# Kernel tuning notes

Hardware: AMD Instinct MI355X
Metric: run time of the kernel (lower is better)

Reference implementation:

```python
import jax, jax.numpy as jnp
import numpy as np

N = 8192
D = 512
N_SLICE = 64
K = 8
H = 30 * K  # 240


def _gen_k_slice(rng):
    xx = rng.normal(0.0, 1.0, (N_SLICE, K, D))
    slices = np.zeros((N_SLICE, K, D), dtype=np.float64)
    for i in range(N_SLICE):
        _, _, vh = np.linalg.svd(xx[i], full_matrices=False)
        slices[i] = vh
    return slices.astype(np.float32)


def setup_inputs() -> dict:
    key = jax.random.key(0)
    k1, k2, k3, k4, k5, k6, k7 = jax.random.split(key, 7)
    rng = np.random.default_rng(0)
    # conv weights: PyTorch Conv1d default init ~ U(-s, s), s = 1/sqrt(fan_in)
    s1 = 1.0 / np.sqrt(K)
    s3 = 1.0 / np.sqrt(H)
    return {
        "X": jax.random.normal(k1, (N, D), dtype=jnp.float32),
        "Y": jax.random.normal(k2, (N, D), dtype=jnp.float32),
        "X_noise": jax.random.normal(k3, (N, N_SLICE * K), dtype=jnp.float32),
        "thetas": jnp.asarray(_gen_k_slice(rng)),                     # [S, K, D]
        "W1": jax.random.uniform(k4, (N_SLICE, H, K), jnp.float32, -s1, s1),
        "b1": jax.random.uniform(k5, (N_SLICE, H), jnp.float32, -s1, s1),
        "W3": jax.random.uniform(k6, (N_SLICE, H), jnp.float32, -s3, s3),
        "b3": jax.random.uniform(k7, (N_SLICE,), jnp.float32, -s3, s3),
        "sigma_noise": 0,
    }


def _mlp(sample, W1, b1, W3, b3):
    # sample: [N, S, K] -> grouped 1x1 conv k->H, relu, grouped conv H->1
    h1 = jax.nn.relu(jnp.einsum('nsk,shk->nsh', sample, W1) + b1[None])
    return jnp.einsum('nsh,sh->ns', h1, W3) + b3[None]  # [N, S]


def reference(X, Y, X_noise, thetas, W1, b1, W3, b3, sigma_noise):
    # batched per-slice projections (fuses the n_slice matmul loop)
    x_sample = jnp.einsum('nd,skd->nsk', X, thetas)  # [N, S, K]
    y_sample = jnp.einsum('nd,skd->nsk', Y, thetas)
    if sigma_noise > 0:
        x_sample = x_sample + sigma_noise * X_noise.reshape(X.shape[0], N_SLICE, K)
    pred_x = _mlp(x_sample, W1, b1, W3, b3)  # [N, S]
    pred_y = _mlp(y_sample, W1, b1, W3, b3)
    n_y = pred_y.shape[0]
    ret = jnp.mean(pred_x, axis=0) - jax.nn.logsumexp(
        pred_y - jnp.log(jnp.float32(n_y)), axis=0)
    return jnp.mean(-ret)
```

## Files before the change

### kernel.cpp

```cpp
#include <hip/hip_runtime.h>
#include <hip/hip_bf16.h>

#define NROWS 8192
#define DDIM  512
#define NS    64
#define KK    8
#define HH    240
#define LDA   40
#define SP    136

typedef __attribute__((ext_vector_type(8))) short bf16x8;
typedef __attribute__((ext_vector_type(4))) float f32x4;

__device__ inline ushort f2bf(float x) {
    unsigned u = __float_as_uint(x);
    unsigned r = u + 0x7fffu + ((u >> 16) & 1u);
    return (ushort)(r >> 16);
}

__global__ __launch_bounds__(256)
void pack_w1_kernel(const float* __restrict__ W1, ushort* __restrict__ W1b)
{
    int i = (blockIdx.x * 256 + threadIdx.x) * 4;
    float4 v = *(const float4*)(W1 + i);
    ushort4 o;
    o.x = f2bf(v.x); o.y = f2bf(v.y); o.z = f2bf(v.z); o.w = f2bf(v.w);
    *(ushort4*)(W1b + i) = o;
}

__global__ __launch_bounds__(256, 4)
void proj_mlp_kernel(const float* __restrict__ X,
                     const float* __restrict__ Y,
                     const float* __restrict__ Xn,
                     const float* __restrict__ Th,
                     const ushort* __restrict__ W1b,
                     const float* __restrict__ b1,
                     const float* __restrict__ W3,
                     const float* __restrict__ b3,
                     const float* __restrict__ sig_p,
                     float* __restrict__ px,
                     float* __restrict__ py)
{
    __shared__ __align__(16) char smem[64 * SP * 2];
    ushort* aT = (ushort*)smem;
    ushort* bT = aT + 64 * LDA;
    ushort* sl = (ushort*)smem;

    const int tid  = threadIdx.x;
    const int w    = __builtin_amdgcn_readfirstlane(tid >> 6);
    const int lane = tid & 63;
    const int bx   = blockIdx.x;
    const int by   = blockIdx.y;

    const bool isX = (bx < 128);
    const int  bxl = isX ? bx : (bx - 128);
    const float* srcA = (isX ? X : Y) + (size_t)bxl * 64 * DDIM;
    const float* srcB = Th + (size_t)by * 128 * DDIM;

    f32x4 acc[2][4];
#pragma unroll
    for (int m = 0; m < 2; ++m)
#pragma unroll
        for (int n = 0; n < 4; ++n) acc[m][n] = (f32x4){0.f, 0.f, 0.f, 0.f};

    const int wr  = (w >> 1) * 32;
    const int wc  = (w & 1) * 64;
    const int r16 = lane & 15;
    const int hi4 = lane >> 4;
    const int offA = (wr + r16) * LDA + hi4 * 8;
    const int offB = (wc + r16) * LDA + hi4 * 8;

    float4 ra[2], rb[4];
#pragma unroll
    for (int i = 0; i < 2; ++i) {
        int f = tid + i * 256;
        ra[i] = *(const float4*)(srcA + (size_t)(f >> 3) * DDIM + (f & 7) * 4);
    }
#pragma unroll
    for (int i = 0; i < 4; ++i) {
        int f = tid + i * 256;
        rb[i] = *(const float4*)(srcB + (size_t)(f >> 3) * DDIM + (f & 7) * 4);
    }

#pragma unroll 1
    for (int kt = 0; kt < DDIM / 32; ++kt) {
        __syncthreads();
#pragma unroll
        for (int i = 0; i < 2; ++i) {
            int f = tid + i * 256;
            ushort4 o;
            o.x = f2bf(ra[i].x); o.y = f2bf(ra[i].y);
            o.z = f2bf(ra[i].z); o.w = f2bf(ra[i].w);
            *(ushort4*)(aT + (f >> 3) * LDA + (f & 7) * 4) = o;
        }
#pragma unroll
        for (int i = 0; i < 4; ++i) {
            int f = tid + i * 256;
            ushort4 o;
            o.x = f2bf(rb[i].x); o.y = f2bf(rb[i].y);
            o.z = f2bf(rb[i].z); o.w = f2bf(rb[i].w);
            *(ushort4*)(bT + (f >> 3) * LDA + (f & 7) * 4) = o;
        }
        __syncthreads();

        if (kt + 1 < DDIM / 32) {
            const int k0 = (kt + 1) * 32;
#pragma unroll
            for (int i = 0; i < 2; ++i) {
                int f = tid + i * 256;
                ra[i] = *(const float4*)(srcA + (size_t)(f >> 3) * DDIM + k0 + (f & 7) * 4);
            }
#pragma unroll
            for (int i = 0; i < 4; ++i) {
                int f = tid + i * 256;
                rb[i] = *(const float4*)(srcB + (size_t)(f >> 3) * DDIM + k0 + (f & 7) * 4);
            }
        }

        bf16x8 af[2], bf[4];
#pragma unroll
        for (int m = 0; m < 2; ++m) af[m] = *(const bf16x8*)(aT + offA + m * 16 * LDA);
#pragma unroll
        for (int n = 0; n < 4; ++n) bf[n] = *(const bf16x8*)(bT + offB + n * 16 * LDA);
#pragma unroll
        for (int m = 0; m < 2; ++m)
#pragma unroll
            for (int n = 0; n < 4; ++n)
                acc[m][n] = __builtin_amdgcn_mfma_f32_16x16x32_bf16(af[m], bf[n], acc[m][n], 0, 0, 0);
    }

    const float sig = *sig_p;
    const bool addnoise = (sig > 0.f) && isX;
    const int n0g = bxl * 64;

    __syncthreads();
#pragma unroll
    for (int m = 0; m < 2; ++m)
#pragma unroll
        for (int n = 0; n < 4; ++n) {
            int col = wc + n * 16 + r16;
#pragma unroll
            for (int j = 0; j < 4; ++j) {
                int row = wr + m * 16 + hi4 * 4 + j;
                float v = acc[m][n][j];
                if (addnoise)
                    v = fmaf(sig, Xn[(size_t)(n0g + row) * (NS * KK) + by * 128 + col], v);
                sl[row * SP + col] = f2bf(v);
            }
        }
    __syncthreads();

    float* dst = isX ? px : py;

#pragma unroll 1
    for (int si = 0; si < 4; ++si) {
        const int sloc = w * 4 + si;
        const int s    = by * 16 + sloc;

        bf16x8 a[4];
#pragma unroll
        for (int m = 0; m < 4; ++m) {
            bf16x8 t = {0, 0, 0, 0, 0, 0, 0, 0};
            if (lane < 16)
                t = *(const bf16x8*)(sl + (m * 16 + lane) * SP + sloc * 8);
            a[m] = t;
        }

        float pacc[4][4];
#pragma unroll
        for (int m = 0; m < 4; ++m)
#pragma unroll
            for (int j = 0; j < 4; ++j) pacc[m][j] = 0.f;

        const ushort* w1p = W1b + (size_t)s * HH * KK;
        const float*  b1p = b1 + s * HH;
        const float*  w3p = W3 + s * HH;

#pragma unroll 3
        for (int ht = 0; ht < HH / 16; ++ht) {
            const int h = ht * 16 + r16;
            bf16x8 bfr = {0, 0, 0, 0, 0, 0, 0, 0};
            if (lane < 16)
                bfr = *(const bf16x8*)(w1p + h * 8);
            const float b1v = b1p[h];
            const float w3v = w3p[h];
            const f32x4 z = (f32x4){b1v, b1v, b1v, b1v};
#pragma unroll
            for (int m = 0; m < 4; ++m) {
                f32x4 t = __builtin_amdgcn_mfma_f32_16x16x32_bf16(a[m], bfr, z, 0, 0, 0);
#pragma unroll
                for (int j = 0; j < 4; ++j)
                    pacc[m][j] = fmaf(fmaxf(t[j], 0.f), w3v, pacc[m][j]);
            }
        }

#pragma unroll
        for (int m = 0; m < 4; ++m)
#pragma unroll
            for (int j = 0; j < 4; ++j) {
                float v = pacc[m][j];
                v += __shfl_xor(v, 1);
                v += __shfl_xor(v, 2);
                v += __shfl_xor(v, 4);
                v += __shfl_xor(v, 8);
                pacc[m][j] = v;
            }

        const float b3v = b3[s];
        if (r16 == 0) {
#pragma unroll
            for (int m = 0; m < 4; ++m) {
                float4 o;
                o.x = pacc[m][0] + b3v;
                o.y = pacc[m][1] + b3v;
                o.z = pacc[m][2] + b3v;
                o.w = pacc[m][3] + b3v;
                *(float4*)(dst + (size_t)s * NROWS + n0g + m * 16 + hi4 * 4) = o;
            }
        }
    }
}

__global__ __launch_bounds__(256)
void reduce1_kernel(const float* __restrict__ px,
                    const float* __restrict__ py,
                    float4* __restrict__ part)
{
    const int s = blockIdx.x >> 2;
    const int q = blockIdx.x & 3;
    const int t = threadIdx.x;
    const float* prx = px + (size_t)s * NROWS + q * 2048;
    const float* pry = py + (size_t)s * NROWS + q * 2048;

    float sx = 0.f, m = -1e30f, se = 0.f;
#pragma unroll
    for (int i = 0; i < 8; ++i) {
        int idx = t + i * 256;
        sx += prx[idx];
        float v = pry[idx];
        if (v > m) {
            se = se * __expf(m - v) + 1.f;
            m = v;
        } else {
            se += __expf(v - m);
        }
    }

    __shared__ float smx[256], smm[256], sms[256];
    smx[t] = sx; smm[t] = m; sms[t] = se;
    __syncthreads();
    for (int off = 128; off > 0; off >>= 1) {
        if (t < off) {
            smx[t] += smx[t + off];
            float m1 = smm[t], m2 = smm[t + off];
            float mm = fmaxf(m1, m2);
            sms[t] = sms[t] * __expf(m1 - mm) + sms[t + off] * __expf(m2 - mm);
            smm[t] = mm;
        }
        __syncthreads();
    }
    if (t == 0) part[blockIdx.x] = (float4){smx[0], smm[0], sms[0], 0.f};
}

__global__ __launch_bounds__(64)
void final_kernel(const float4* __restrict__ part, float* __restrict__ out)
{
    const int s = threadIdx.x;
    float sum = 0.f, m = -1e30f, se = 0.f;
#pragma unroll
    for (int q = 0; q < 4; ++q) {
        float4 p = part[s * 4 + q];
        sum += p.x;
        float mm = fmaxf(m, p.y);
        se = se * __expf(m - mm) + p.z * __expf(p.y - mm);
        m = mm;
    }
    float lse  = m + logf(se);
    float term = lse - logf((float)NROWS) - sum / (float)NROWS;
#pragma unroll
    for (int off = 32; off > 0; off >>= 1) term += __shfl_down(term, off);
    if (s == 0) out[0] = term * (1.0f / (float)NS);
}

extern "C" void kernel_launch(void* const* d_in, const int* in_sizes, int n_in,
                              void* d_out, int out_size, void* d_ws, size_t ws_size,
                              hipStream_t stream)
{
    const float* X   = (const float*)d_in[0];
    const float* Y   = (const float*)d_in[1];
    const float* Xn  = (const float*)d_in[2];
    const float* Th  = (const float*)d_in[3];
    const float* W1  = (const float*)d_in[4];
    const float* b1  = (const float*)d_in[5];
    const float* W3  = (const float*)d_in[6];
    const float* b3  = (const float*)d_in[7];
    const float* sig = (const float*)d_in[8];

    float*  px   = (float*)d_ws;
    float*  py   = px + (size_t)NS * NROWS;
    ushort* W1b  = (ushort*)(py + (size_t)NS * NROWS);
    float4* part = (float4*)(W1b + (size_t)NS * HH * KK);

    pack_w1_kernel<<<NS * HH * KK / 1024, 256, 0, stream>>>(W1, W1b);

    dim3 g1(256, 4, 1);
    proj_mlp_kernel<<<g1, 256, 0, stream>>>(X, Y, Xn, Th, W1b, b1, W3, b3,
                                            sig, px, py);
    reduce1_kernel<<<256, 256, 0, stream>>>(px, py, part);
    final_kernel<<<1, 64, 0, stream>>>(part, (float*)d_out);
}
```

Baseline: 73.18 us.

## Fuse per-block reductions into MLP kernel, deepen K tile, transpose MLP MFMA

After: 79.80 us. +9.0%, slower.

```diff
diff --git a/kernel.cpp b/kernel.cpp
--- a/kernel.cpp
+++ b/kernel.cpp
@@ -6,11 +6,12 @@
 #define NS    64
 #define KK    8
 #define HH    240
-#define LDA   40
+#define LDB   72
 #define SP    136
 
 typedef __attribute__((ext_vector_type(8))) short bf16x8;
 typedef __attribute__((ext_vector_type(4))) float f32x4;
+typedef __attribute__((ext_vector_type(2))) float f32x2;
 
 __device__ inline ushort f2bf(float x) {
     unsigned u = __float_as_uint(x);
@@ -36,14 +37,14 @@
                      const ushort* __restrict__ W1b,
                      const float* __restrict__ b1,
                      const float* __restrict__ W3,
-                     const float* __restrict__ b3,
                      const float* __restrict__ sig_p,
-                     float* __restrict__ px,
-                     float* __restrict__ py)
-{
-    __shared__ __align__(16) char smem[64 * SP * 2];
+                     float* __restrict__ sumx,
+                     float* __restrict__ maxy,
+                     float* __restrict__ sey)
+{
+    __shared__ __align__(16) char smem[(64 + 128) * LDB * 2];
     ushort* aT = (ushort*)smem;
-    ushort* bT = aT + 64 * LDA;
+    ushort* bT = aT + 64 * LDB;
     ushort* sl = (ushort*)smem;
 
     const int tid  = threadIdx.x;
@@ -67,66 +68,71 @@
     const int wc  = (w & 1) * 64;
     const int r16 = lane & 15;
     const int hi4 = lane >> 4;
-    const int offA = (wr + r16) * LDA + hi4 * 8;
-    const int offB = (wc + r16) * LDA + hi4 * 8;
-
-    float4 ra[2], rb[4];
-#pragma unroll
-    for (int i = 0; i < 2; ++i) {
-        int f = tid + i * 256;
-        ra[i] = *(const float4*)(srcA + (size_t)(f >> 3) * DDIM + (f & 7) * 4);
-    }
+    const int offA = (wr + r16) * LDB + hi4 * 8;
+    const int offB = (wc + r16) * LDB + hi4 * 8;
+
+    float4 ra[4], rb[8];
 #pragma unroll
     for (int i = 0; i < 4; ++i) {
         int f = tid + i * 256;
-        rb[i] = *(const float4*)(srcB + (size_t)(f >> 3) * DDIM + (f & 7) * 4);
+        ra[i] = *(const float4*)(srcA + (size_t)(f >> 4) * DDIM + (f & 15) * 4);
+    }
+#pragma unroll
+    for (int i = 0; i < 8; ++i) {
+        int f = tid + i * 256;
+        rb[i] = *(const float4*)(srcB + (size_t)(f >> 4) * DDIM + (f & 15) * 4);
     }
 
 #pragma unroll 1
-    for (int kt = 0; kt < DDIM / 32; ++kt) {
+    for (int kt = 0; kt < DDIM / 64; ++kt) {
         __syncthreads();
 #pragma unroll
-        for (int i = 0; i < 2; ++i) {
+        for (int i = 0; i < 4; ++i) {
             int f = tid + i * 256;
             ushort4 o;
             o.x = f2bf(ra[i].x); o.y = f2bf(ra[i].y);
             o.z = f2bf(ra[i].z); o.w = f2bf(ra[i].w);
-            *(ushort4*)(aT + (f >> 3) * LDA + (f & 7) * 4) = o;
-        }
-#pragma unroll
-        for (int i = 0; i < 4; ++i) {
+            *(ushort4*)(aT + (f >> 4) * LDB + (f & 15) * 4) = o;
+        }
+#pragma unroll
+        for (int i = 0; i < 8; ++i) {
             int f = tid + i * 256;
             ushort4 o;
             o.x = f2bf(rb[i].x); o.y = f2bf(rb[i].y);
             o.z = f2bf(rb[i].z); o.w = f2bf(rb[i].w);
-            *(ushort4*)(bT + (f >> 3) * LDA + (f & 7) * 4) = o;
+            *(ushort4*)(bT + (f >> 4) * LDB + (f & 15) * 4) = o;
         }
         __syncthreads();
 
-        if (kt + 1 < DDIM / 32) {
-            const int k0 = (kt + 1) * 32;
-#pragma unroll
-            for (int i = 0; i < 2; ++i) {
-                int f = tid + i * 256;
-                ra[i] = *(const float4*)(srcA + (size_t)(f >> 3) * DDIM + k0 + (f & 7) * 4);
-            }
+        if (kt + 1 < DDIM / 64) {
+            const int k0 = (kt + 1) * 64;
 #pragma unroll
             for (int i = 0; i < 4; ++i) {
                 int f = tid + i * 256;
-                rb[i] = *(const float4*)(srcB + (size_t)(f >> 3) * DDIM + k0 + (f & 7) * 4);
-            }
-        }
-
-        bf16x8 af[2], bf[4];
-#pragma unroll
-        for (int m = 0; m < 2; ++m) af[m] = *(const bf16x8*)(aT + offA + m * 16 * LDA);
-#pragma unroll
-        for (int n = 0; n < 4; ++n) bf[n] = *(const bf16x8*)(bT + offB + n * 16 * LDA);
-#pragma unroll
-        for (int m = 0; m < 2; ++m)
+                ra[i] = *(const float4*)(srcA + (size_t)(f >> 4) * DDIM + k0 + (f & 15) * 4);
+            }
+#pragma unroll
+            for (int i = 0; i < 8; ++i) {
+                int f = tid + i * 256;
+                rb[i] = *(const float4*)(srcB + (size_t)(f >> 4) * DDIM + k0 + (f & 15) * 4);
+            }
+        }
+
+#pragma unroll
+        for (int ks = 0; ks < 2; ++ks) {
+            bf16x8 af[2], bf[4];
+#pragma unroll
+            for (int m = 0; m < 2; ++m)
+                af[m] = *(const bf16x8*)(aT + offA + m * 16 * LDB + ks * 32);
 #pragma unroll
             for (int n = 0; n < 4; ++n)
-                acc[m][n] = __builtin_amdgcn_mfma_f32_16x16x32_bf16(af[m], bf[n], acc[m][n], 0, 0, 0);
+                bf[n] = *(const bf16x8*)(bT + offB + n * 16 * LDB + ks * 32);
+#pragma unroll
+            for (int m = 0; m < 2; ++m)
+#pragma unroll
+                for (int n = 0; n < 4; ++n)
+                    acc[m][n] = __builtin_amdgcn_mfma_f32_16x16x32_bf16(af[m], bf[n], acc[m][n], 0, 0, 0);
+        }
     }
 
     const float sig = *sig_p;
@@ -150,135 +156,115 @@
         }
     __syncthreads();
 
-    float* dst = isX ? px : py;
-
 #pragma unroll 1
     for (int si = 0; si < 4; ++si) {
         const int sloc = w * 4 + si;
         const int s    = by * 16 + sloc;
 
-        bf16x8 a[4];
-#pragma unroll
-        for (int m = 0; m < 4; ++m) {
+        bf16x8 bsamp[4];
+#pragma unroll
+        for (int nt = 0; nt < 4; ++nt) {
             bf16x8 t = {0, 0, 0, 0, 0, 0, 0, 0};
-            if (lane < 16)
-                t = *(const bf16x8*)(sl + (m * 16 + lane) * SP + sloc * 8);
-            a[m] = t;
-        }
-
-        float pacc[4][4];
-#pragma unroll
-        for (int m = 0; m < 4; ++m)
-#pragma unroll
-            for (int j = 0; j < 4; ++j) pacc[m][j] = 0.f;
+            if (hi4 == 0)
+                t = *(const bf16x8*)(sl + (nt * 16 + r16) * SP + sloc * 8);
+            bsamp[nt] = t;
+        }
 
         const ushort* w1p = W1b + (size_t)s * HH * KK;
         const float*  b1p = b1 + s * HH;
         const float*  w3p = W3 + s * HH;
 
-#pragma unroll 3
+        f32x2 pn2[4];
+#pragma unroll
+        for (int nt = 0; nt < 4; ++nt) pn2[nt] = (f32x2){0.f, 0.f};
+
+#pragma unroll 5
         for (int ht = 0; ht < HH / 16; ++ht) {
-            const int h = ht * 16 + r16;
-            bf16x8 bfr = {0, 0, 0, 0, 0, 0, 0, 0};
-            if (lane < 16)
-                bfr = *(const bf16x8*)(w1p + h * 8);
-            const float b1v = b1p[h];
-            const float w3v = w3p[h];
-            const f32x4 z = (f32x4){b1v, b1v, b1v, b1v};
-#pragma unroll
-            for (int m = 0; m < 4; ++m) {
-                f32x4 t = __builtin_amdgcn_mfma_f32_16x16x32_bf16(a[m], bfr, z, 0, 0, 0);
-#pragma unroll
-                for (int j = 0; j < 4; ++j)
-                    pacc[m][j] = fmaf(fmaxf(t[j], 0.f), w3v, pacc[m][j]);
-            }
-        }
-
-#pragma unroll
-        for (int m = 0; m < 4; ++m)
-#pragma unroll
-            for (int j = 0; j < 4; ++j) {
-                float v = pacc[m][j];
-                v += __shfl_xor(v, 1);
-                v += __shfl_xor(v, 2);
-                v += __shfl_xor(v, 4);
-                v += __shfl_xor(v, 8);
-                pacc[m][j] = v;
-            }
-
-        const float b3v = b3[s];
-        if (r16 == 0) {
-#pragma unroll
-            for (int m = 0; m < 4; ++m) {
-                float4 o;
-                o.x = pacc[m][0] + b3v;
-                o.y = pacc[m][1] + b3v;
-                o.z = pacc[m][2] + b3v;
-                o.w = pacc[m][3] + b3v;
-                *(float4*)(dst + (size_t)s * NROWS + n0g + m * 16 + hi4 * 4) = o;
-            }
-        }
-    }
-}
-
-__global__ __launch_bounds__(256)
-void reduce1_kernel(const float* __restrict__ px,
-                    const float* __restrict__ py,
-                    float4* __restrict__ part)
-{
-    const int s = blockIdx.x >> 2;
-    const int q = blockIdx.x & 3;
-    const int t = threadIdx.x;
-    const float* prx = px + (size_t)s * NROWS + q * 2048;
-    const float* pry = py + (size_t)s * NROWS + q * 2048;
-
-    float sx = 0.f, m = -1e30f, se = 0.f;
-#pragma unroll
-    for (int i = 0; i < 8; ++i) {
-        int idx = t + i * 256;
-        sx += prx[idx];
-        float v = pry[idx];
-        if (v > m) {
-            se = se * __expf(m - v) + 1.f;
-            m = v;
+            bf16x8 aw = {0, 0, 0, 0, 0, 0, 0, 0};
+            if (hi4 == 0)
+                aw = *(const bf16x8*)(w1p + (ht * 16 + r16) * 8);
+            float4 b4 = *(const float4*)(b1p + ht * 16 + hi4 * 4);
+            float4 w4 = *(const float4*)(w3p + ht * 16 + hi4 * 4);
+            f32x4 z = (f32x4){b4.x, b4.y, b4.z, b4.w};
+            f32x2 w01 = (f32x2){w4.x, w4.y};
+            f32x2 w23 = (f32x2){w4.z, w4.w};
+            const f32x2 zero2 = (f32x2){0.f, 0.f};
+#pragma unroll
+            for (int nt = 0; nt < 4; ++nt) {
+                f32x4 t = __builtin_amdgcn_mfma_f32_16x16x32_bf16(aw, bsamp[nt], z, 0, 0, 0);
+                f32x2 t01 = (f32x2){t[0], t[1]};
+                f32x2 t23 = (f32x2){t[2], t[3]};
+                t01 = __builtin_elementwise_max(t01, zero2);
+                t23 = __builtin_elementwise_max(t23, zero2);
+                pn2[nt] = __builtin_elementwise_fma(t01, w01, pn2[nt]);
+                pn2[nt] = __builtin_elementwise_fma(t23, w23, pn2[nt]);
+            }
+        }
+
+        if (isX) {
+            float lsum = 0.f;
+#pragma unroll
+            for (int nt = 0; nt < 4; ++nt) lsum += pn2[nt].x + pn2[nt].y;
+#pragma unroll
+            for (int off = 1; off < 64; off <<= 1)
+                lsum += __shfl_xor(lsum, off);
+            if (lane == 0) sumx[s * 128 + bxl] = lsum;
         } else {
-            se += __expf(v - m);
-        }
-    }
-
-    __shared__ float smx[256], smm[256], sms[256];
-    smx[t] = sx; smm[t] = m; sms[t] = se;
-    __syncthreads();
-    for (int off = 128; off > 0; off >>= 1) {
-        if (t < off) {
-            smx[t] += smx[t + off];
-            float m1 = smm[t], m2 = smm[t + off];
-            float mm = fmaxf(m1, m2);
-            sms[t] = sms[t] * __expf(m1 - mm) + sms[t + off] * __expf(m2 - mm);
-            smm[t] = mm;
-        }
-        __syncthreads();
-    }
-    if (t == 0) part[blockIdx.x] = (float4){smx[0], smm[0], sms[0], 0.f};
+            float p[4];
+#pragma unroll
+            for (int nt = 0; nt < 4; ++nt) {
+                f32x2 v = pn2[nt];
+                v.x += __shfl_xor(v.x, 16);
+                v.y += __shfl_xor(v.y, 16);
+                v.x += __shfl_xor(v.x, 32);
+                v.y += __shfl_xor(v.y, 32);
+                p[nt] = v.x + v.y;
+            }
+            float M = fmaxf(fmaxf(p[0], p[1]), fmaxf(p[2], p[3]));
+            float se = __expf(p[0] - M) + __expf(p[1] - M)
+                     + __expf(p[2] - M) + __expf(p[3] - M);
+#pragma unroll
+            for (int off = 1; off < 16; off <<= 1) {
+                float Mo = __shfl_xor(M, off);
+                float so = __shfl_xor(se, off);
+                float Mm = fmaxf(M, Mo);
+                se = se * __expf(M - Mm) + so * __expf(Mo - Mm);
+                M = Mm;
+            }
+            if (lane == 0) {
+                maxy[s * 128 + bxl] = M;
+                sey[s * 128 + bxl]  = se;
+            }
+        }
+    }
 }
 
 __global__ __launch_bounds__(64)
-void final_kernel(const float4* __restrict__ part, float* __restrict__ out)
+void final_kernel(const float* __restrict__ sumx,
+                  const float* __restrict__ maxy,
+                  const float* __restrict__ sey,
+                  float* __restrict__ out)
 {
     const int s = threadIdx.x;
-    float sum = 0.f, m = -1e30f, se = 0.f;
-#pragma unroll
-    for (int q = 0; q < 4; ++q) {
-        float4 p = part[s * 4 + q];
-        sum += p.x;
-        float mm = fmaxf(m, p.y);
-        se = se * __expf(m - mm) + p.z * __expf(p.y - mm);
-        m = mm;
-    }
-    float lse  = m + logf(se);
-    float term = lse - logf((float)NROWS) - sum / (float)NROWS;
-#pragma unroll
-    for (int off = 32; off > 0; off >>= 1) term += __shfl_down(term, off);
+    const float* sxp = sumx + s * 128;
+    const float* myp = maxy + s * 128;
+    const float* sep = sey + s * 128;
+
+    float sum = 0.f, M = -3.4e38f;
+#pragma unroll 8
+    for (int i = 0; i < 128; ++i) {
+        sum += sxp[i];
+        M = fmaxf(M, myp[i]);
+    }
+    float se = 0.f;
+#pragma unroll 8
+    for (int i = 0; i < 128; ++i)
+        se += sep[i] * __expf(myp[i] - M);
+
+    float lse  = M + logf(se);
+    float term = lse - logf((float)NROWS) - sum * (1.0f / (float)NROWS);
+#pragma unroll
+    for (int off = 1; off < 64; off <<= 1) term += __shfl_xor(term, off);
     if (s == 0) out[0] = term * (1.0f / (float)NS);
 }
 
@@ -293,19 +279,17 @@
     const float* W1  = (const float*)d_in[4];
     const float* b1  = (const float*)d_in[5];
     const float* W3  = (const float*)d_in[6];
-    const float* b3  = (const float*)d_in[7];
     const float* sig = (const float*)d_in[8];
 
-    float*  px   = (float*)d_ws;
-    float*  py   = px + (size_t)NS * NROWS;
-    ushort* W1b  = (ushort*)(py + (size_t)NS * NROWS);
-    float4* part = (float4*)(W1b + (size_t)NS * HH * KK);
+    ushort* W1b  = (ushort*)d_ws;
+    float*  sumx = (float*)((char*)d_ws + (size_t)NS * HH * KK * 2);
+    float*  maxy = sumx + NS * 128;
+    float*  sey  = maxy + NS * 128;
 
     pack_w1_kernel<<<NS * HH * KK / 1024, 256, 0, stream>>>(W1, W1b);
 
     dim3 g1(256, 4, 1);
-    proj_mlp_kernel<<<g1, 256, 0, stream>>>(X, Y, Xn, Th, W1b, b1, W3, b3,
-                                            sig, px, py);
-    reduce1_kernel<<<256, 256, 0, stream>>>(px, py, part);
-    final_kernel<<<1, 64, 0, stream>>>(part, (float*)d_out);
-}
+    proj_mlp_kernel<<<g1, 256, 0, stream>>>(X, Y, Xn, Th, W1b, b1, W3,
+                                            sig, sumx, maxy, sey);
+    final_kernel<<<1, 64, 0, stream>>>(sumx, maxy, sey, (float*)d_out);
+}
```
